# Kernel tuning notes

Hardware: AMD Instinct MI355X
Metric: run time of the kernel (lower is better)

Reference implementation:

```python
import jax, jax.numpy as jnp
import numpy as np

N_NODES = 100000
N_EDGES = 3200000
N_GRAPHS = 256
DIMS = [11, 200, 200, 200, 200, 200]  # acfg_init_dims + cfg_filters
CONCAT = sum(DIMS[1:])  # 1000


def setup_inputs() -> dict:
    key = jax.random.key(0)
    ks = jax.random.split(key, 32)
    d = {}
    d["x"] = jax.random.normal(ks[0], (N_NODES, DIMS[0]), jnp.float32)
    d["edge_index"] = jax.random.randint(ks[1], (2, N_EDGES), 0, N_NODES)
    d["batch"] = jnp.sort(jax.random.randint(ks[2], (N_NODES,), 0, N_GRAPHS))
    ki = 3
    # SAGEConv params: lin_l (neighbors, with bias) + lin_r (root, no bias)
    for i in range(5):
        fi, fo = DIMS[i], DIMS[i + 1]
        s = 1.0 / np.sqrt(fi)
        d[f"Wl{i+1}"] = jax.random.uniform(ks[ki], (fo, fi), jnp.float32, -s, s); ki += 1
        d[f"bl{i+1}"] = jnp.zeros((fo,), jnp.float32)
        d[f"Wr{i+1}"] = jax.random.uniform(ks[ki], (fo, fi), jnp.float32, -s, s); ki += 1
    # projection head 1000 -> 500 -> 250 -> 1
    for j, (fi, fo) in enumerate([(CONCAT, CONCAT // 2), (CONCAT // 2, CONCAT // 4), (CONCAT // 4, 1)]):
        s = 1.0 / np.sqrt(fi)
        d[f"pw{j+1}"] = jax.random.uniform(ks[ki], (fo, fi), jnp.float32, -s, s); ki += 1
        d[f"pb{j+1}"] = jnp.zeros((fo,), jnp.float32)
    return d


def reference(x, edge_index, batch,
              Wl1, bl1, Wr1, Wl2, bl2, Wr2, Wl3, bl3, Wr3,
              Wl4, bl4, Wr4, Wl5, bl5, Wr5,
              pw1, pb1, pw2, pb2, pw3, pb3):
    src, dst = edge_index[0], edge_index[1]
    # in-degree for mean aggregation (computed once, reused by all layers)
    deg = jax.ops.segment_sum(jnp.ones((src.shape[0],), x.dtype), dst, N_NODES)
    inv_deg = (1.0 / jnp.maximum(deg, 1.0))[:, None]

    def sage(h, Wl, bl, Wr):
        agg = jax.ops.segment_sum(h[src], dst, N_NODES) * inv_deg  # mean of neighbor feats
        return agg @ Wl.T + bl + h @ Wr.T

    layers = [(Wl1, bl1, Wr1), (Wl2, bl2, Wr2), (Wl3, bl3, Wr3), (Wl4, bl4, Wr4), (Wl5, bl5, Wr5)]
    h = x
    outs = []
    for Wl, bl, Wr in layers:
        h = jax.nn.relu(sage(h, Wl, bl, Wr))
        outs.append(h)
    hc = jnp.concatenate(outs, axis=1)  # [N, 1000]

    # global_mean_pool over graph ids
    cnt = jax.ops.segment_sum(jnp.ones((x.shape[0],), x.dtype), batch, N_GRAPHS)
    g = jax.ops.segment_sum(hc, batch, N_GRAPHS) / jnp.maximum(cnt, 1.0)[:, None]

    # dropout is identity in eval mode (functional.dropout with training=False)
    g = g @ pw1.T + pb1
    g = g @ pw2.T + pb2
    g = g @ pw3.T + pb3  # [num_graphs, 1]
    return jax.nn.sigmoid(g).squeeze(1)
```

## Files before the change

kernel.cpp:

```cpp
#include <hip/hip_runtime.h>
#include <math.h>

typedef __attribute__((ext_vector_type(4))) float floatx4;
typedef __attribute__((ext_vector_type(2))) float floatx2;

#define ROWP 256
#define R4   16
#define NT 14
#define NTC 13
#define KS 7
#define PACK_BYTES (NT*KS*64*8)
#define PACK1_BYTES (NT*64*8)
#define STAGE_BYTES (NTC*KS*64*8)
#define BSHIFT 6
#define EPB 4096
#define MAXBUCK 1600
#define PT_STRIDE 208

__device__ __forceinline__ unsigned short f2bf(float f){
    union { float f; unsigned u; } v; v.f = f;
    unsigned r = v.u + 0x7FFF + ((v.u >> 16) & 1);
    return (unsigned short)(r >> 16);
}
__device__ __forceinline__ unsigned pk4_fp8(float a, float b, float c, float d){
    int w = __builtin_amdgcn_cvt_pk_fp8_f32(a, b, 0, false);
    w = __builtin_amdgcn_cvt_pk_fp8_f32(c, d, w, true);
    return (unsigned)w;
}
__device__ __forceinline__ unsigned char b1_fp8(float a){
    int w = __builtin_amdgcn_cvt_pk_fp8_f32(a, a, 0, false);
    return (unsigned char)(w & 0xFF);
}


__global__ __launch_bounds__(256) void k_bin_hist(
    const int* __restrict__ dst, int* __restrict__ hist, int E, int nbuck)
{
    __shared__ int lh[MAXBUCK];
    for (int i = threadIdx.x; i < nbuck; i += 256) lh[i] = 0;
    __syncthreads();
    int base = blockIdx.x * EPB;
    #pragma unroll
    for (int k = 0; k < EPB / 256; ++k){
        int e = base + k * 256 + threadIdx.x;
        if (e < E) atomicAdd(&lh[dst[e] >> BSHIFT], 1);
    }
    __syncthreads();
    for (int i = threadIdx.x; i < nbuck; i += 256)
        hist[(size_t)blockIdx.x * nbuck + i] = lh[i];
}

__global__ __launch_bounds__(256) void k_col_scan(
    int* __restrict__ hist, int* __restrict__ T, int nblk, int nbuck)
{
    __shared__ int part[4][64];
    int w = threadIdx.x >> 6, l = threadIdx.x & 63;
    int b = blockIdx.x * 64 + l;
    int chunk = (nblk + 3) >> 2;
    int j0 = w * chunk, j1 = j0 + chunk; if (j1 > nblk) j1 = nblk;
    int s = 0;
    if (b < nbuck)
        for (int j = j0; j < j1; ++j) s += hist[(size_t)j * nbuck + b];
    part[w][l] = s;
    __syncthreads();
    if (b < nbuck){
        int run = 0;
        for (int w2 = 0; w2 < w; ++w2) run += part[w2][l];
        for (int j = j0; j < j1; ++j){
            int v = hist[(size_t)j * nbuck + b];
            hist[(size_t)j * nbuck + b] = run;
            run += v;
        }
        if (w == 3) T[b] = part[0][l] + part[1][l] + part[2][l] + part[3][l];
    }
}

__global__ __launch_bounds__(256) void k_scan_t(
    const int* __restrict__ T, int* __restrict__ tbase, int nbuck)
{
    __shared__ int ts[256];
    int t = threadIdx.x;
    int v[8]; int s = 0;
    int base = t * 8;
    #pragma unroll
    for (int k = 0; k < 8; ++k){
        int idx = base + k;
        v[k] = (idx < nbuck) ? T[idx] : 0;
        s += v[k];
    }
    ts[t] = s; __syncthreads();
    #pragma unroll
    for (int off = 1; off < 256; off <<= 1){
        int p = (t >= off) ? ts[t - off] : 0;
        __syncthreads();
        ts[t] += p;
        __syncthreads();
    }
    int run = ts[t] - s;
    #pragma unroll
    for (int k = 0; k < 8; ++k){
        int idx = base + k;
        if (idx < nbuck) tbase[idx] = run;
        run += v[k];
    }
    if (t == 255) tbase[nbuck] = ts[255];
}

__global__ __launch_bounds__(256) void k_bin_scatter(
    const int* __restrict__ src, const int* __restrict__ dst,
    const int* __restrict__ off, const int* __restrict__ tbase,
    unsigned* __restrict__ pairs, int E, int nbuck)
{
    __shared__ int lbase[MAXBUCK];
    __shared__ int lc[MAXBUCK];
    for (int i = threadIdx.x; i < nbuck; i += 256){
        lbase[i] = off[(size_t)blockIdx.x * nbuck + i] + tbase[i];
        lc[i] = 0;
    }
    __syncthreads();
    int base = blockIdx.x * EPB;
    #pragma unroll
    for (int k = 0; k < EPB / 256; ++k){
        int e = base + k * 256 + threadIdx.x;
        if (e < E){
            int d = dst[e];
            int b = d >> BSHIFT;
            int r = atomicAdd(&lc[b], 1);
            pairs[lbase[b] + r] = ((unsigned)(d & 63) << 26) | (unsigned)src[e];
        }
    }
}

__global__ __launch_bounds__(256) void k_bucket_deg(
    const unsigned* __restrict__ pairs, const int* __restrict__ tbase,
    int* __restrict__ deg, float* __restrict__ inv_deg, int N)
{
    __shared__ int ld[64];
    int b = blockIdx.x;
    if (threadIdx.x < 64) ld[threadIdx.x] = 0;
    __syncthreads();
    int pb = tbase[b], pe = tbase[b + 1];
    for (int e = pb + threadIdx.x; e < pe; e += 256)
        atomicAdd(&ld[pairs[e] >> 26], 1);
    __syncthreads();
    if (threadIdx.x < 64){
        int node = (b << BSHIFT) + threadIdx.x;
        if (node < N){
            int d = ld[threadIdx.x];
            deg[node] = d;
            inv_deg[node] = 1.0f / fmaxf((float)d, 1.0f);
        }
    }
}

__global__ __launch_bounds__(256) void k_place(
    const unsigned* __restrict__ pairs, const int* __restrict__ tbase,
    const int* __restrict__ row_ptr, int* __restrict__ srcs, int N)
{
    __shared__ int lrp[64];
    __shared__ int lcur[64];
    int b = blockIdx.x;
    if (threadIdx.x < 64){
        int node = (b << BSHIFT) + threadIdx.x;
        lrp[threadIdx.x] = (node < N) ? row_ptr[node] : 0;
        lcur[threadIdx.x] = 0;
    }
    __syncthreads();
    int pb = tbase[b], pe = tbase[b + 1];
    for (int e = pb + threadIdx.x; e < pe; e += 256){
        unsigned pr = pairs[e];
        int li = pr >> 26;
        int r = atomicAdd(&lcur[li], 1);
        srcs[lrp[li] + r] = (int)(pr & 0x03FFFFFFu);
    }
}


__global__ void k_scan_sums(const int* __restrict__ deg, int* __restrict__ csum, int N){
    __shared__ int sd[256];
    int base = blockIdx.x * 1024;
    int s = 0;
    for (int i = threadIdx.x; i < 1024; i += 256){
        int idx = base + i;
        s += (idx < N) ? deg[idx] : 0;
    }
    sd[threadIdx.x] = s; __syncthreads();
    for (int off = 128; off > 0; off >>= 1){
        if (threadIdx.x < off) sd[threadIdx.x] += sd[threadIdx.x + off];
        __syncthreads();
    }
    if (threadIdx.x == 0) csum[blockIdx.x] = sd[0];
}

__global__ void k_scan_apply(const int* __restrict__ deg, const int* __restrict__ csum,
                             int* __restrict__ row_ptr, int N, int E, int nchunks){
    __shared__ int ts[256];
    __shared__ int base_s;
    int partial = 0;
    for (int j = threadIdx.x; j < nchunks; j += 256)
        if (j < (int)blockIdx.x) partial += csum[j];
    ts[threadIdx.x] = partial; __syncthreads();
    for (int off = 128; off > 0; off >>= 1){
        if (threadIdx.x < off) ts[threadIdx.x] += ts[threadIdx.x + off];
        __syncthreads();
    }
    if (threadIdx.x == 0) base_s = ts[0];
    __syncthreads();
    int blk_base = base_s;
    __syncthreads();

    int base = blockIdx.x * 1024 + threadIdx.x * 4;
    int v[4]; int s = 0;
    #pragma unroll
    for (int j = 0; j < 4; ++j){
        int idx = base + j;
        v[j] = (idx < N) ? deg[idx] : 0;
        s += v[j];
    }
    ts[threadIdx.x] = s; __syncthreads();
    #pragma unroll
    for (int off = 1; off < 256; off <<= 1){
        int t = (threadIdx.x >= off) ? ts[threadIdx.x - off] : 0;
        __syncthreads();
        ts[threadIdx.x] += t;
        __syncthreads();
    }
    int excl = ts[threadIdx.x] - s + blk_base;
    #pragma unroll
    for (int j = 0; j < 4; ++j){
        int idx = base + j;
        if (idx < N) row_ptr[idx] = excl;
        excl += v[j];
    }
    if (blockIdx.x == 0 && threadIdx.x == 0) row_ptr[N] = E;
}


__global__ void k_gstart_bs(const int* __restrict__ batch, int* __restrict__ gstart,
                            int N, int NG){
    int g = blockIdx.x * blockDim.x + threadIdx.x;
    if (g > NG) return;
    int lo = 0, hi = N;
    while (lo < hi){
        int mid = (lo + hi) >> 1;
        if (batch[mid] < g) lo = mid + 1; else hi = mid;
    }
    gstart[g] = lo;
}


__global__ void k_pack_w(const float* W0, const float* W1, const float* W2, const float* W3,
                         const float* W4, const float* W5, const float* W6, const float* W7,
                         unsigned char* __restrict__ out){
    const float* Ws[8] = {W0,W1,W2,W3,W4,W5,W6,W7};
    const float* W = Ws[blockIdx.z];
    int lane = threadIdx.x;
    int n  = blockIdx.x * 16 + (lane & 15);
    int k0 = blockIdx.y * 32 + (lane >> 4) * 8;
    float f[8];
    #pragma unroll
    for (int j = 0; j < 8; ++j){
        int k = k0 + j;
        f[j] = (n < 200 && k < 200) ? W[n * 200 + k] : 0.f;
    }
    uint2 u;
    u.x = pk4_fp8(f[0], f[1], f[2], f[3]);
    u.y = pk4_fp8(f[4], f[5], f[6], f[7]);
    size_t off = ((((size_t)blockIdx.z * NT + blockIdx.x) * KS + blockIdx.y) * 64 + lane) * 8;
    *reinterpret_cast<uint2*>(out + off) = u;
}

__global__ __launch_bounds__(256) void k_pack_misc(
    const float* __restrict__ x, unsigned short* __restrict__ xp,
    unsigned char* __restrict__ xa,
    const float* __restrict__ Wl1, const float* __restrict__ Wr1,
    unsigned char* __restrict__ w1pack,
    const float* b0, const float* b1, const float* b2, const float* b3, const float* b4,
    float* __restrict__ biasp, int N, int xblk)
{
    int bid = blockIdx.x;
    if (bid < xblk){
        int i = bid * 256 + threadIdx.x;
        int node = i >> 4, c = i & 15;
        if (node < N){
            float f = (c < 11) ? x[(size_t)node * 11 + c] : 0.f;
            xp[i] = f2bf(f);
            xa[(size_t)node * 32 + 16 + c] = b1_fp8(f);
        }
        return;
    }
    int j = bid - xblk;
    if (j < NT){
        if (threadIdx.x >= 64) return;
        int lane = threadIdx.x;
        int n  = j * 16 + (lane & 15);
        int k0 = (lane >> 4) * 8;
        float f[8];
        #pragma unroll
        for (int jj = 0; jj < 8; ++jj){
            int k = k0 + jj;
            float v = 0.f;
            if (n < 200){
                if (k < 11)                 v = Wl1[n * 11 + k];
                else if (k >= 16 && k < 27) v = Wr1[n * 11 + (k - 16)];
            }
            f[jj] = v;
        }
        uint2 u;
        u.x = pk4_fp8(f[0], f[1], f[2], f[3]);
        u.y = pk4_fp8(f[4], f[5], f[6], f[7]);
        size_t off = ((size_t)j * 64 + lane) * 8;
        *reinterpret_cast<uint2*>(w1pack + off) = u;
        return;
    }
    int l = j - NT;
    const float* bs[5] = {b0,b1,b2,b3,b4};
    int c = threadIdx.x;
    if (c < ROWP) biasp[l * ROWP + c] = (c < 200) ? bs[l][c] : 0.f;
}


__global__ __launch_bounds__(256) void k_agg11(
    const unsigned short* __restrict__ xp, const int* __restrict__ row_ptr,
    const int* __restrict__ srcs, const float* __restrict__ inv_deg,
    unsigned char* __restrict__ xa, int N)
{
    int half = threadIdx.x >> 5;
    int node = blockIdx.x * 8 + half;
    int l = threadIdx.x & 31;
    if (node >= N) return;
    int beg = row_ptr[node], end = row_ptr[node + 1];

    float acc[12];
    #pragma unroll
    for (int i = 0; i < 12; ++i) acc[i] = 0.f;

    const uint4* x4 = reinterpret_cast<const uint4*>(xp);
    const uint2* x2 = reinterpret_cast<const uint2*>(xp);
    for (int e = beg + l; e < end; e += 32){
        int sn = srcs[e];
        uint4 a = x4[(size_t)sn * 2];
        uint2 b = x2[(size_t)sn * 4 + 2];
        union { unsigned u; float f; } c;
        c.u = a.x << 16;         acc[0] += c.f;
        c.u = a.x & 0xffff0000u; acc[1] += c.f;
        c.u = a.y << 16;         acc[2] += c.f;
        c.u = a.y & 0xffff0000u; acc[3] += c.f;
        c.u = a.z << 16;         acc[4] += c.f;
        c.u = a.z & 0xffff0000u; acc[5] += c.f;
        c.u = a.w << 16;         acc[6] += c.f;
        c.u = a.w & 0xffff0000u; acc[7] += c.f;
        c.u = b.x << 16;         acc[8] += c.f;
        c.u = b.x & 0xffff0000u; acc[9] += c.f;
        c.u = b.y << 16;         acc[10] += c.f;
        c.u = b.y & 0xffff0000u; acc[11] += c.f;
    }

    #pragma unroll
    for (int i = 0; i < 11; ++i){
        acc[i] += __shfl_xor(acc[i], 1, 64);
        acc[i] += __shfl_xor(acc[i], 2, 64);
        acc[i] += __shfl_xor(acc[i], 4, 64);
        acc[i] += __shfl_xor(acc[i], 8, 64);
        acc[i] += __shfl_xor(acc[i], 16, 64);
    }

    if (l == 0){
        float id = inv_deg[node];
        float v[12];
        #pragma unroll
        for (int i = 0; i < 11; ++i) v[i] = acc[i] * id;
        v[11] = 0.f;
        uint4 o;
        o.x = pk4_fp8(v[0], v[1], v[2], v[3]);
        o.y = pk4_fp8(v[4], v[5], v[6], v[7]);
        o.z = pk4_fp8(v[8], v[9], v[10], v[11]);
        o.w = 0u;
        *reinterpret_cast<uint4*>(xa + (size_t)node * 32) = o;
    }
}


__device__ __forceinline__ void accum_fp8v(floatx2* a, uint4 u){
    a[0] += __builtin_amdgcn_cvt_pk_f32_fp8((int)u.x, false);
    a[1] += __builtin_amdgcn_cvt_pk_f32_fp8((int)u.x, true );
    a[2] += __builtin_amdgcn_cvt_pk_f32_fp8((int)u.y, false);
    a[3] += __builtin_amdgcn_cvt_pk_f32_fp8((int)u.y, true );
    a[4] += __builtin_amdgcn_cvt_pk_f32_fp8((int)u.z, false);
    a[5] += __builtin_amdgcn_cvt_pk_f32_fp8((int)u.z, true );
    a[6] += __builtin_amdgcn_cvt_pk_f32_fp8((int)u.w, false);
    a[7] += __builtin_amdgcn_cvt_pk_f32_fp8((int)u.w, true );
}

__global__ __launch_bounds__(256) void k_agg200(
    const unsigned char* __restrict__ h8, const int* __restrict__ row_ptr,
    const int* __restrict__ srcs, const float* __restrict__ inv_deg,
    unsigned char* __restrict__ agg, int N)
{
    int node = blockIdx.x * 4 + (threadIdx.x >> 6);
    int lane = threadIdx.x & 63;
    if (node >= N) return;
    int g = lane >> 4;
    int l = lane & 15;
    int beg = row_ptr[node], end = row_ptr[node + 1];
    int nb = end - beg;

    floatx2 acc[8];
    #pragma unroll
    for (int i = 0; i < 8; ++i) acc[i] = (floatx2){0.f, 0.f};

    const uint4* h4 = reinterpret_cast<const uint4*>(h8);

    for (int t = 0; t < nb; t += 64){
        int cnt = nb - t; if (cnt > 64) cnt = 64;
        int eidx = t + lane;
        int si = srcs[beg + (eidx < nb ? eidx : nb - 1)];
        int jmax = (cnt - g + 3) >> 2;

        int j = 0;
        for (; j + 4 <= jmax; j += 4){
            int b0 = g + 4 * j;
            int s0 = __shfl(si, b0,      64);
            int s1 = __shfl(si, b0 + 4,  64);
            int s2 = __shfl(si, b0 + 8,  64);
            int s3 = __shfl(si, b0 + 12, 64);
            uint4 u0 = h4[(size_t)s0 * R4 + l];
            uint4 u1 = h4[(size_t)s1 * R4 + l];
            uint4 u2 = h4[(size_t)s2 * R4 + l];
            uint4 u3 = h4[(size_t)s3 * R4 + l];
            accum_fp8v(acc, u0);
            accum_fp8v(acc, u1);
            accum_fp8v(acc, u2);
            accum_fp8v(acc, u3);
        }
        for (; j < jmax; ++j){
            int s0 = __shfl(si, g + 4 * j, 64);
            uint4 u0 = h4[(size_t)s0 * R4 + l];
            accum_fp8v(acc, u0);
        }
    }

    float af[16];
    #pragma unroll
    for (int i = 0; i < 8; ++i){ af[2*i] = acc[i][0]; af[2*i+1] = acc[i][1]; }
    #pragma unroll
    for (int i = 0; i < 16; ++i){
        af[i] += __shfl_xor(af[i], 32, 64);
        af[i] += __shfl_xor(af[i], 16, 64);
    }

    if (g == 0){
        float id = inv_deg[node];
        uint4 o;
        o.x = pk4_fp8(af[0] * id,  af[1] * id,  af[2] * id,  af[3] * id);
        o.y = pk4_fp8(af[4] * id,  af[5] * id,  af[6] * id,  af[7] * id);
        o.z = pk4_fp8(af[8] * id,  af[9] * id,  af[10] * id, af[11] * id);
        o.w = pk4_fp8(af[12] * id, af[13] * id, af[14] * id, af[15] * id);
        *reinterpret_cast<uint4*>(agg + (size_t)node * ROWP + l * 16) = o;
    }
}


__global__ __launch_bounds__(256) void k_layer1_mfma(
    const unsigned char* __restrict__ xa, const unsigned char* __restrict__ W1p,
    const float* __restrict__ biasp, const int* __restrict__ batch,
    float* __restrict__ gsum, unsigned char* __restrict__ outp, int M)
{
    __shared__ __align__(16) unsigned char ptile[64 * PT_STRIDE];
    __shared__ int lb[64];
    const int wave = threadIdx.x >> 6;
    const int lane = threadIdx.x & 63;
    const int n = lane & 15;
    const int q = lane >> 4;
    const int r0 = blockIdx.x * 64;
    const int nrows = (M - r0 < 64) ? (M - r0) : 64;
    int row = r0 + wave * 16 + n;
    int rowc = row < M ? row : (M - 1);

    if (threadIdx.x < 64 && threadIdx.x < nrows) lb[threadIdx.x] = batch[r0 + threadIdx.x];

    long a = *reinterpret_cast<const long*>(xa + (size_t)rowc * 32 + q * 8);

    floatx4 acc[NTC];
    #pragma unroll
    for (int nt = 0; nt < NTC; ++nt){
        long b = *reinterpret_cast<const long*>(W1p + ((size_t)nt * 64 + lane) * 8);
        acc[nt] = __builtin_amdgcn_mfma_f32_16x16x32_fp8_fp8(a, b, (floatx4){0.f,0.f,0.f,0.f}, 0, 0, 0);
    }

    {
        int lr0 = wave * 16 + q * 4;
        #pragma unroll
        for (int nt = 0; nt < NTC; ++nt){
            float bsv = biasp[nt * 16 + n];
            #pragma unroll
            for (int r = 0; r < 4; ++r){
                float v = fmaxf(acc[nt][r] + bsv, 0.f);
                ptile[(lr0 + r) * PT_STRIDE + nt * 16 + n] = b1_fp8(v);
            }
        }
    }
    __syncthreads();

    {
        const uint4* s4 = reinterpret_cast<const uint4*>(ptile);
        int tot = nrows * 13;
        for (int i = threadIdx.x; i < tot; i += 256){
            int r = i / 13, c = i - r * 13;
            *reinterpret_cast<uint4*>(outp + (size_t)(r0 + r) * ROWP + c * 16) = s4[i];
        }
    }

    if (threadIdx.x < 50){
        int t = threadIdx.x;
        const unsigned* pd = reinterpret_cast<const unsigned*>(ptile);
        float s0 = 0.f, s1 = 0.f, s2 = 0.f, s3 = 0.f;
        int cur = lb[0];
        for (int r = 0; r < nrows; ++r){
            int gg = lb[r];
            if (gg != cur){
                float* gp = &gsum[(size_t)cur * 1000 + t * 4];
                atomicAdd(gp + 0, s0); atomicAdd(gp + 1, s1);
                atomicAdd(gp + 2, s2); atomicAdd(gp + 3, s3);
                s0 = s1 = s2 = s3 = 0.f;
                cur = gg;
            }
            unsigned u = pd[r * 52 + t];
            floatx2 lo = __builtin_amdgcn_cvt_pk_f32_fp8((int)u, false);
            floatx2 hi = __builtin_amdgcn_cvt_pk_f32_fp8((int)u, true);
            s0 += lo[0]; s1 += lo[1]; s2 += hi[0]; s3 += hi[1];
        }
        float* gp = &gsum[(size_t)cur * 1000 + t * 4];
        atomicAdd(gp + 0, s0); atomicAdd(gp + 1, s1);
        atomicAdd(gp + 2, s2); atomicAdd(gp + 3, s3);
    }
}

__global__ __launch_bounds__(256) void k_sage_mfma(
    const unsigned char* __restrict__ Aagg, const unsigned char* __restrict__ Ah,
    const unsigned char* __restrict__ Wlp, const unsigned char* __restrict__ Wrp,
    const float* __restrict__ biasp, const int* __restrict__ batch,
    float* __restrict__ gsum, int col_off,
    unsigned char* __restrict__ outp, int M)
{
    __shared__ __align__(16) unsigned char lw[STAGE_BYTES];
    __shared__ int lb[64];
    const int wave = threadIdx.x >> 6;
    const int lane = threadIdx.x & 63;
    const int n = lane & 15;
    const int q = lane >> 4;
    const int r0 = blockIdx.x * 64;
    const int nrows = (M - r0 < 64) ? (M - r0) : 64;
    int row = r0 + wave * 16 + n;
    int rowc = row < M ? row : (M - 1);

    if (threadIdx.x < 64 && threadIdx.x < nrows) lb[threadIdx.x] = batch[r0 + threadIdx.x];

    floatx4 acc[NTC];
    #pragma unroll
    for (int nt = 0; nt < NTC; ++nt) acc[nt] = (floatx4){0.f, 0.f, 0.f, 0.f};

    const unsigned char* Wp[2] = {Wlp, Wrp};
    const unsigned char* Ap[2] = {Aagg, Ah};

    #pragma unroll
    for (int phase = 0; phase < 2; ++phase){
        if (phase) __syncthreads();
        {
            const uint4* src4 = reinterpret_cast<const uint4*>(Wp[phase]);
            uint4* dst4 = reinterpret_cast<uint4*>(lw);
            for (int i = threadIdx.x; i < STAGE_BYTES / 16; i += 256)
                dst4[i] = src4[i];
        }
        __syncthreads();

        const unsigned char* arow = Ap[phase] + (size_t)rowc * ROWP + q * 8;
        long a[KS];
        #pragma unroll
        for (int ks = 0; ks < 6; ++ks)
            a[ks] = *reinterpret_cast<const long*>(arow + ks * 32);
        a[6] = (q < 2) ? *reinterpret_cast<const long*>(arow + 192) : 0L;

        #pragma unroll
        for (int ks = 0; ks < KS; ++ks){
            #pragma unroll
            for (int nt = 0; nt < NTC; ++nt){
                long b = *reinterpret_cast<const long*>(&lw[((nt * KS + ks) * 64 + lane) * 8]);
                acc[nt] = __builtin_amdgcn_mfma_f32_16x16x32_fp8_fp8(a[ks], b, acc[nt], 0, 0, 0);
            }
        }
    }
    __syncthreads();

    unsigned char* ptile = lw;
    {
        int lr0 = wave * 16 + q * 4;
        #pragma unroll
        for (int nt = 0; nt < NTC; ++nt){
            float bsv = biasp[nt * 16 + n];
            #pragma unroll
            for (int r = 0; r < 4; ++r){
                float v = fmaxf(acc[nt][r] + bsv, 0.f);
                ptile[(lr0 + r) * PT_STRIDE + nt * 16 + n] = b1_fp8(v);
            }
        }
    }
    __syncthreads();

    {
        const uint4* s4 = reinterpret_cast<const uint4*>(ptile);
        int tot = nrows * 13;
        for (int i = threadIdx.x; i < tot; i += 256){
            int r = i / 13, c = i - r * 13;
            *reinterpret_cast<uint4*>(outp + (size_t)(r0 + r) * ROWP + c * 16) = s4[i];
        }
    }

    if (threadIdx.x < 50){
        int t = threadIdx.x;
        const unsigned* pd = reinterpret_cast<const unsigned*>(ptile);
        float s0 = 0.f, s1 = 0.f, s2 = 0.f, s3 = 0.f;
        int cur = lb[0];
        for (int r = 0; r < nrows; ++r){
            int gg = lb[r];
            if (gg != cur){
                float* gp = &gsum[(size_t)cur * 1000 + col_off + t * 4];
                atomicAdd(gp + 0, s0); atomicAdd(gp + 1, s1);
                atomicAdd(gp + 2, s2); atomicAdd(gp + 3, s3);
                s0 = s1 = s2 = s3 = 0.f;
                cur = gg;
            }
            unsigned u = pd[r * 52 + t];
            floatx2 lo = __builtin_amdgcn_cvt_pk_f32_fp8((int)u, false);
            floatx2 hi = __builtin_amdgcn_cvt_pk_f32_fp8((int)u, true);
            s0 += lo[0]; s1 += lo[1]; s2 += hi[0]; s3 += hi[1];
        }
        float* gp = &gsum[(size_t)cur * 1000 + col_off + t * 4];
        atomicAdd(gp + 0, s0); atomicAdd(gp + 1, s1);
        atomicAdd(gp + 2, s2); atomicAdd(gp + 3, s3);
    }
}


__global__ __launch_bounds__(256) void k_mlp_first(
    const float* __restrict__ gsum, const int* __restrict__ gstart,
    const float* __restrict__ W, const float* __restrict__ b,
    float* __restrict__ outp)
{
    __shared__ __align__(16) float row[1000];
    int g = blockIdx.x;
    int cnt = gstart[g+1] - gstart[g];
    float inv = 1.0f / fmaxf((float)cnt, 1.0f);
    for (int i = threadIdx.x; i < 1000; i += 256)
        row[i] = gsum[(size_t)g * 1000 + i] * inv;
    __syncthreads();
    for (int c = threadIdx.x; c < 500; c += 256){
        const float4* w4 = reinterpret_cast<const float4*>(W + (size_t)c * 1000);
        const float4* r4 = reinterpret_cast<const float4*>(row);
        float s = b[c];
        for (int k = 0; k < 250; ++k){
            float4 wv = w4[k]; float4 rv = r4[k];
            s = fmaf(wv.x, rv.x, s);
            s = fmaf(wv.y, rv.y, s);
            s = fmaf(wv.z, rv.z, s);
            s = fmaf(wv.w, rv.w, s);
        }
        outp[(size_t)g * 500 + c] = s;
    }
}

__global__ __launch_bounds__(256) void k_mlp23(
    const float* __restrict__ t1, const float* __restrict__ W2,
    const float* __restrict__ b2, const float* __restrict__ W3,
    const float* __restrict__ b3, float* __restrict__ outp)
{
    __shared__ __align__(16) float row[500];
    __shared__ float red[256];
    int g = blockIdx.x;
    for (int i = threadIdx.x; i < 500; i += 256) row[i] = t1[(size_t)g * 500 + i];
    __syncthreads();
    float prod = 0.f;
    int c = threadIdx.x;
    if (c < 250){
        const float4* w4 = reinterpret_cast<const float4*>(W2 + (size_t)c * 500);
        const float4* r4 = reinterpret_cast<const float4*>(row);
        float s = b2[c];
        for (int k = 0; k < 125; ++k){
            float4 wv = w4[k]; float4 rv = r4[k];
            s = fmaf(wv.x, rv.x, s);
            s = fmaf(wv.y, rv.y, s);
            s = fmaf(wv.z, rv.z, s);
            s = fmaf(wv.w, rv.w, s);
        }
        prod = s * W3[c];
    }
    red[threadIdx.x] = prod;
    __syncthreads();
    for (int off = 128; off > 0; off >>= 1){
        if (threadIdx.x < off) red[threadIdx.x] += red[threadIdx.x + off];
        __syncthreads();
    }
    if (threadIdx.x == 0)
        outp[g] = 1.0f / (1.0f + expf(-(red[0] + b3[0])));
}


extern "C" void kernel_launch(void* const* d_in, const int* in_sizes, int n_in,
                              void* d_out, int out_size, void* d_ws, size_t ws_size,
                              hipStream_t stream)
{
    const float* x    = (const float*)d_in[0];
    const int*   ei   = (const int*)d_in[1];
    const int*   batch= (const int*)d_in[2];
    const float* Wl[5]; const float* bl[5]; const float* Wr[5];
    for (int i = 0; i < 5; ++i){
        Wl[i] = (const float*)d_in[3 + 3*i];
        bl[i] = (const float*)d_in[4 + 3*i];
        Wr[i] = (const float*)d_in[5 + 3*i];
    }
    const float* pw1 = (const float*)d_in[18]; const float* pb1 = (const float*)d_in[19];
    const float* pw2 = (const float*)d_in[20]; const float* pb2 = (const float*)d_in[21];
    const float* pw3 = (const float*)d_in[22]; const float* pb3 = (const float*)d_in[23];
    float* out = (float*)d_out;

    const int N  = in_sizes[2];
    const int E  = in_sizes[1] / 2;
    const int NG = out_size;
    const int* esrc = ei;
    const int* edst = ei + E;
    const int nbuck = (N + 63) >> BSHIFT;
    const int nblk  = (E + EPB - 1) / EPB;

    char* p = (char*)d_ws;
    auto carve = [&](size_t bytes)->void* {
        void* r = (void*)p;
        p += (bytes + 255) & ~(size_t)255;
        return r;
    };
    int*   deg     = (int*)  carve((size_t)N * 4);
    int*   row_ptr = (int*)  carve(((size_t)N + 1) * 4);
    int*   csum    = (int*)  carve(4096);
    int*   hist    = (int*)  carve((size_t)nblk * nbuck * 4);
    int*   Tb      = (int*)  carve((size_t)nbuck * 4);
    int*   tbase   = (int*)  carve(((size_t)nbuck + 1) * 4);
    float* invdeg  = (float*)carve((size_t)N * 4);
    int*   gstart  = (int*)  carve(((size_t)NG + 1) * 4);
    int*   srcs    = (int*)  carve((size_t)E * 4);
    unsigned* pairs = (unsigned*)carve((size_t)E * 4);
    unsigned short* xp    = (unsigned short*)carve((size_t)N * 16 * 2);
    unsigned char*  xa    = (unsigned char*) carve((size_t)N * 32);
    unsigned char*  agg8  = (unsigned char*) carve((size_t)N * ROWP);
    unsigned char*  h8A   = (unsigned char*) carve((size_t)N * ROWP);
    unsigned char*  h8B   = (unsigned char*) carve((size_t)N * ROWP);
    unsigned char*  wpack = (unsigned char*) carve((size_t)8 * PACK_BYTES);
    unsigned char*  w1pack= (unsigned char*) carve((size_t)PACK1_BYTES);
    float* biasp   = (float*)carve((size_t)5 * ROWP * 4);
    float* gsum    = (float*)carve((size_t)NG * 1000 * 4);
    float* t1      = (float*)carve((size_t)NG * 500 * 4);

    hipMemsetAsync(gsum, 0, (size_t)NG * 1000 * 4, stream);
    hipMemsetAsync(h8A, 0, (size_t)N * ROWP, stream);
    hipMemsetAsync(h8B, 0, (size_t)N * ROWP, stream);

    int xblk = (N * 16 + 255) / 256;
    k_pack_w<<<dim3(NT, KS, 8), 64, 0, stream>>>(
        Wl[1], Wr[1], Wl[2], Wr[2], Wl[3], Wr[3], Wl[4], Wr[4], wpack);
    k_pack_misc<<<xblk + NT + 5, 256, 0, stream>>>(
        x, xp, xa, Wl[0], Wr[0], w1pack,
        bl[0], bl[1], bl[2], bl[3], bl[4], biasp, N, xblk);

    k_bin_hist<<<nblk, 256, 0, stream>>>(edst, hist, E, nbuck);
    k_col_scan<<<(nbuck + 63) / 64, 256, 0, stream>>>(hist, Tb, nblk, nbuck);
    k_scan_t<<<1, 256, 0, stream>>>(Tb, tbase, nbuck);
    k_bin_scatter<<<nblk, 256, 0, stream>>>(esrc, edst, hist, tbase, pairs, E, nbuck);
    k_bucket_deg<<<nbuck, 256, 0, stream>>>(pairs, tbase, deg, invdeg, N);
    int nchunks = (N + 1023) / 1024;
    k_scan_sums<<<nchunks, 256, 0, stream>>>(deg, csum, N);
    k_scan_apply<<<nchunks, 256, 0, stream>>>(deg, csum, row_ptr, N, E, nchunks);
    k_place<<<nbuck, 256, 0, stream>>>(pairs, tbase, row_ptr, srcs, N);

    k_gstart_bs<<<(NG + 256) / 256, 256, 0, stream>>>(batch, gstart, N, NG);

    int gb = (N + 63) / 64;
    k_agg11<<<(N + 7) / 8, 256, 0, stream>>>(xp, row_ptr, srcs, invdeg, xa, N);
    k_layer1_mfma<<<gb, 256, 0, stream>>>(xa, w1pack, biasp, batch, gsum, h8A, N);

    unsigned char* hc = h8A; unsigned char* hn = h8B;
    int ab = (N + 3) / 4;
    for (int L = 1; L < 5; ++L){
        k_agg200<<<ab, 256, 0, stream>>>(hc, row_ptr, srcs, invdeg, agg8, N);
        const unsigned char* Wlp = wpack + (size_t)((L-1)*2 + 0) * PACK_BYTES;
        const unsigned char* Wrp = wpack + (size_t)((L-1)*2 + 1) * PACK_BYTES;
        k_sage_mfma<<<gb, 256, 0, stream>>>(agg8, hc, Wlp, Wrp,
                                            biasp + L * ROWP, batch, gsum, 200 * L,
                                            hn, N);
        k_pool_dummy:;
        unsigned char* t = hc; hc = hn; hn = t;
    }

    k_mlp_first<<<NG, 256, 0, stream>>>(gsum, gstart, pw1, pb1, t1);
    k_mlp23<<<NG, 256, 0, stream>>>(t1, pw2, pb2, pw3, pb3, out);
}
```

Baseline: 1.110 ms.

## Split fp8 feature rows into two 128-byte column planes for aggregation

Node feature and aggregate buffers move from one 256-byte row per node to two planes of 128 bytes each. Neighbor aggregation now runs as two launches, one per plane, with 8 lanes per edge and 8 edges in flight per wave instead of 16 and 4. The aim is a smaller gather working set per launch so more of it stays in cache. In exchange, `srcs`/`row_ptr` are read twice, there is an extra launch and reduction step, and the MFMA kernel now loads unmasked padding columns in plane 1.

```diff
diff --git a/kernel.cpp b/kernel.cpp
--- a/kernel.cpp
+++ b/kernel.cpp
@@ -5,7 +5,6 @@
 typedef __attribute__((ext_vector_type(2))) float floatx2;
 
 #define ROWP 256
-#define R4   16
 #define NT 14
 #define NTC 13
 #define KS 7
@@ -16,6 +15,7 @@
 #define EPB 4096
 #define MAXBUCK 1600
 #define PT_STRIDE 208
+
 
 __device__ __forceinline__ unsigned short f2bf(float f){
     union { float f; unsigned u; } v; v.f = f;
@@ -392,16 +392,16 @@
     a[7] += __builtin_amdgcn_cvt_pk_f32_fp8((int)u.w, true );
 }
 
-__global__ __launch_bounds__(256) void k_agg200(
-    const unsigned char* __restrict__ h8, const int* __restrict__ row_ptr,
+__global__ __launch_bounds__(256) void k_agg200h(
+    const unsigned char* __restrict__ hpl, const int* __restrict__ row_ptr,
     const int* __restrict__ srcs, const float* __restrict__ inv_deg,
-    unsigned char* __restrict__ agg, int N)
+    unsigned char* __restrict__ aggpl, int N)
 {
     int node = blockIdx.x * 4 + (threadIdx.x >> 6);
     int lane = threadIdx.x & 63;
     if (node >= N) return;
-    int g = lane >> 4;
-    int l = lane & 15;
+    int g = lane >> 3;
+    int l = lane & 7;
     int beg = row_ptr[node], end = row_ptr[node + 1];
     int nb = end - beg;
 
@@ -409,33 +409,33 @@
     #pragma unroll
     for (int i = 0; i < 8; ++i) acc[i] = (floatx2){0.f, 0.f};
 
-    const uint4* h4 = reinterpret_cast<const uint4*>(h8);
+    const uint4* h4 = reinterpret_cast<const uint4*>(hpl);
 
     for (int t = 0; t < nb; t += 64){
         int cnt = nb - t; if (cnt > 64) cnt = 64;
         int eidx = t + lane;
         int si = srcs[beg + (eidx < nb ? eidx : nb - 1)];
-        int jmax = (cnt - g + 3) >> 2;
+        int jmax = (cnt - g + 7) >> 3;
 
         int j = 0;
         for (; j + 4 <= jmax; j += 4){
-            int b0 = g + 4 * j;
+            int b0 = g + 8 * j;
             int s0 = __shfl(si, b0,      64);
-            int s1 = __shfl(si, b0 + 4,  64);
-            int s2 = __shfl(si, b0 + 8,  64);
-            int s3 = __shfl(si, b0 + 12, 64);
-            uint4 u0 = h4[(size_t)s0 * R4 + l];
-            uint4 u1 = h4[(size_t)s1 * R4 + l];
-            uint4 u2 = h4[(size_t)s2 * R4 + l];
-            uint4 u3 = h4[(size_t)s3 * R4 + l];
+            int s1 = __shfl(si, b0 + 8,  64);
+            int s2 = __shfl(si, b0 + 16, 64);
+            int s3 = __shfl(si, b0 + 24, 64);
+            uint4 u0 = h4[(size_t)s0 * 8 + l];
+            uint4 u1 = h4[(size_t)s1 * 8 + l];
+            uint4 u2 = h4[(size_t)s2 * 8 + l];
+            uint4 u3 = h4[(size_t)s3 * 8 + l];
             accum_fp8v(acc, u0);
             accum_fp8v(acc, u1);
             accum_fp8v(acc, u2);
             accum_fp8v(acc, u3);
         }
         for (; j < jmax; ++j){
-            int s0 = __shfl(si, g + 4 * j, 64);
-            uint4 u0 = h4[(size_t)s0 * R4 + l];
+            int s0 = __shfl(si, g + 8 * j, 64);
+            uint4 u0 = h4[(size_t)s0 * 8 + l];
             accum_fp8v(acc, u0);
         }
     }
@@ -445,8 +445,9 @@
     for (int i = 0; i < 8; ++i){ af[2*i] = acc[i][0]; af[2*i+1] = acc[i][1]; }
     #pragma unroll
     for (int i = 0; i < 16; ++i){
+        af[i] += __shfl_xor(af[i], 8, 64);
+        af[i] += __shfl_xor(af[i], 16, 64);
         af[i] += __shfl_xor(af[i], 32, 64);
-        af[i] += __shfl_xor(af[i], 16, 64);
     }
 
     if (g == 0){
@@ -456,7 +457,7 @@
         o.y = pk4_fp8(af[4] * id,  af[5] * id,  af[6] * id,  af[7] * id);
         o.z = pk4_fp8(af[8] * id,  af[9] * id,  af[10] * id, af[11] * id);
         o.w = pk4_fp8(af[12] * id, af[13] * id, af[14] * id, af[15] * id);
-        *reinterpret_cast<uint4*>(agg + (size_t)node * ROWP + l * 16) = o;
+        *reinterpret_cast<uint4*>(aggpl + (size_t)node * 128 + l * 16) = o;
     }
 }
 
@@ -503,11 +504,16 @@
     __syncthreads();
 
     {
+        unsigned char* out0 = outp;
+        unsigned char* out1 = outp + (size_t)M * 128;
         const uint4* s4 = reinterpret_cast<const uint4*>(ptile);
         int tot = nrows * 13;
         for (int i = threadIdx.x; i < tot; i += 256){
             int r = i / 13, c = i - r * 13;
-            *reinterpret_cast<uint4*>(outp + (size_t)(r0 + r) * ROWP + c * 16) = s4[i];
+            unsigned char* dst = (c < 8)
+                ? out0 + (size_t)(r0 + r) * 128 + c * 16
+                : out1 + (size_t)(r0 + r) * 128 + (c - 8) * 16;
+            *reinterpret_cast<uint4*>(dst) = s4[i];
         }
     }
 
@@ -562,6 +568,7 @@
 
     const unsigned char* Wp[2] = {Wlp, Wrp};
     const unsigned char* Ap[2] = {Aagg, Ah};
+    const size_t plane = (size_t)M * 128;
 
     #pragma unroll
     for (int phase = 0; phase < 2; ++phase){
@@ -574,12 +581,15 @@
         }
         __syncthreads();
 
-        const unsigned char* arow = Ap[phase] + (size_t)rowc * ROWP + q * 8;
+        const unsigned char* A0 = Ap[phase] + (size_t)rowc * 128 + q * 8;
+        const unsigned char* A1 = A0 + plane;
         long a[KS];
         #pragma unroll
-        for (int ks = 0; ks < 6; ++ks)
-            a[ks] = *reinterpret_cast<const long*>(arow + ks * 32);
-        a[6] = (q < 2) ? *reinterpret_cast<const long*>(arow + 192) : 0L;
+        for (int ks = 0; ks < 4; ++ks)
+            a[ks] = *reinterpret_cast<const long*>(A0 + ks * 32);
+        #pragma unroll
+        for (int ks = 4; ks < KS; ++ks)
+            a[ks] = *reinterpret_cast<const long*>(A1 + (ks - 4) * 32);
 
         #pragma unroll
         for (int ks = 0; ks < KS; ++ks){
@@ -608,11 +618,16 @@
     __syncthreads();
 
     {
+        unsigned char* out0 = outp;
+        unsigned char* out1 = outp + plane;
         const uint4* s4 = reinterpret_cast<const uint4*>(ptile);
         int tot = nrows * 13;
         for (int i = threadIdx.x; i < tot; i += 256){
             int r = i / 13, c = i - r * 13;
-            *reinterpret_cast<uint4*>(outp + (size_t)(r0 + r) * ROWP + c * 16) = s4[i];
+            unsigned char* dst = (c < 8)
+                ? out0 + (size_t)(r0 + r) * 128 + c * 16
+                : out1 + (size_t)(r0 + r) * 128 + (c - 8) * 16;
+            *reinterpret_cast<uint4*>(dst) = s4[i];
         }
     }
 
@@ -787,14 +802,15 @@
 
     unsigned char* hc = h8A; unsigned char* hn = h8B;
     int ab = (N + 3) / 4;
+    size_t plane = (size_t)N * 128;
     for (int L = 1; L < 5; ++L){
-        k_agg200<<<ab, 256, 0, stream>>>(hc, row_ptr, srcs, invdeg, agg8, N);
+        k_agg200h<<<ab, 256, 0, stream>>>(hc,         row_ptr, srcs, invdeg, agg8,         N);
+        k_agg200h<<<ab, 256, 0, stream>>>(hc + plane, row_ptr, srcs, invdeg, agg8 + plane, N);
         const unsigned char* Wlp = wpack + (size_t)((L-1)*2 + 0) * PACK_BYTES;
         const unsigned char* Wrp = wpack + (size_t)((L-1)*2 + 1) * PACK_BYTES;
         k_sage_mfma<<<gb, 256, 0, stream>>>(agg8, hc, Wlp, Wrp,
                                             biasp + L * ROWP, batch, gsum, 200 * L,
                                             hn, N);
-        k_pool_dummy:;
         unsigned char* t = hc; hc = hn; hn = t;
     }
 
```

Measured after the change: 1.389 ms. +25.1%, slower.

## Split node features into 32-byte column planes and gather per slice

Applied to the files above, without the earlier changes.

Stores the fp8 node feature rows as eight planes of 32 bytes per node instead of one 256-byte row. The aggregation kernel now gives each block one plane for 128 nodes and two threads per node, each walking that node's neighbor list on its own, instead of one wave per node with shuffles. The aim is a smaller gather working set per plane and no cross-lane reductions. In exchange it adds thread divergence from uneven degrees and gathers an eighth plane that is not needed. It also reads padding bytes that are never written and that the old code explicitly zeroed.

```diff
diff --git a/kernel.cpp b/kernel.cpp
--- a/kernel.cpp
+++ b/kernel.cpp
@@ -5,7 +5,6 @@
 typedef __attribute__((ext_vector_type(2))) float floatx2;
 
 #define ROWP 256
-#define R4   16
 #define NT 14
 #define NTC 13
 #define KS 7
@@ -16,6 +15,7 @@
 #define EPB 4096
 #define MAXBUCK 1600
 #define PT_STRIDE 208
+
 
 __device__ __forceinline__ unsigned short f2bf(float f){
     union { float f; unsigned u; } v; v.f = f;
@@ -392,72 +392,53 @@
     a[7] += __builtin_amdgcn_cvt_pk_f32_fp8((int)u.w, true );
 }
 
-__global__ __launch_bounds__(256) void k_agg200(
-    const unsigned char* __restrict__ h8, const int* __restrict__ row_ptr,
+__global__ __launch_bounds__(256) void k_agg200s(
+    const unsigned char* __restrict__ hpl, const int* __restrict__ row_ptr,
     const int* __restrict__ srcs, const float* __restrict__ inv_deg,
-    unsigned char* __restrict__ agg, int N)
-{
-    int node = blockIdx.x * 4 + (threadIdx.x >> 6);
-    int lane = threadIdx.x & 63;
+    unsigned char* __restrict__ aggpl, int N)
+{
+    const int s    = blockIdx.x & 7;
+    const int nb0  = (blockIdx.x >> 3) * 128;
+    const int grp  = threadIdx.x >> 1;
+    const int half = threadIdx.x & 1;
+    const int node = nb0 + grp;
     if (node >= N) return;
-    int g = lane >> 4;
-    int l = lane & 15;
+    const size_t plane = (size_t)N * 32;
+    const uint4* h4 = reinterpret_cast<const uint4*>(hpl + (size_t)s * plane);
     int beg = row_ptr[node], end = row_ptr[node + 1];
-    int nb = end - beg;
 
     floatx2 acc[8];
     #pragma unroll
     for (int i = 0; i < 8; ++i) acc[i] = (floatx2){0.f, 0.f};
 
-    const uint4* h4 = reinterpret_cast<const uint4*>(h8);
-
-    for (int t = 0; t < nb; t += 64){
-        int cnt = nb - t; if (cnt > 64) cnt = 64;
-        int eidx = t + lane;
-        int si = srcs[beg + (eidx < nb ? eidx : nb - 1)];
-        int jmax = (cnt - g + 3) >> 2;
-
-        int j = 0;
-        for (; j + 4 <= jmax; j += 4){
-            int b0 = g + 4 * j;
-            int s0 = __shfl(si, b0,      64);
-            int s1 = __shfl(si, b0 + 4,  64);
-            int s2 = __shfl(si, b0 + 8,  64);
-            int s3 = __shfl(si, b0 + 12, 64);
-            uint4 u0 = h4[(size_t)s0 * R4 + l];
-            uint4 u1 = h4[(size_t)s1 * R4 + l];
-            uint4 u2 = h4[(size_t)s2 * R4 + l];
-            uint4 u3 = h4[(size_t)s3 * R4 + l];
-            accum_fp8v(acc, u0);
-            accum_fp8v(acc, u1);
-            accum_fp8v(acc, u2);
-            accum_fp8v(acc, u3);
-        }
-        for (; j < jmax; ++j){
-            int s0 = __shfl(si, g + 4 * j, 64);
-            uint4 u0 = h4[(size_t)s0 * R4 + l];
-            accum_fp8v(acc, u0);
-        }
-    }
-
-    float af[16];
-    #pragma unroll
-    for (int i = 0; i < 8; ++i){ af[2*i] = acc[i][0]; af[2*i+1] = acc[i][1]; }
-    #pragma unroll
-    for (int i = 0; i < 16; ++i){
-        af[i] += __shfl_xor(af[i], 32, 64);
-        af[i] += __shfl_xor(af[i], 16, 64);
-    }
-
-    if (g == 0){
-        float id = inv_deg[node];
-        uint4 o;
-        o.x = pk4_fp8(af[0] * id,  af[1] * id,  af[2] * id,  af[3] * id);
-        o.y = pk4_fp8(af[4] * id,  af[5] * id,  af[6] * id,  af[7] * id);
-        o.z = pk4_fp8(af[8] * id,  af[9] * id,  af[10] * id, af[11] * id);
-        o.w = pk4_fp8(af[12] * id, af[13] * id, af[14] * id, af[15] * id);
-        *reinterpret_cast<uint4*>(agg + (size_t)node * ROWP + l * 16) = o;
-    }
+    int e = beg;
+    for (; e + 4 <= end; e += 4){
+        int s0 = srcs[e];
+        int s1 = srcs[e + 1];
+        int s2 = srcs[e + 2];
+        int s3 = srcs[e + 3];
+        uint4 u0 = h4[(size_t)s0 * 2 + half];
+        uint4 u1 = h4[(size_t)s1 * 2 + half];
+        uint4 u2 = h4[(size_t)s2 * 2 + half];
+        uint4 u3 = h4[(size_t)s3 * 2 + half];
+        accum_fp8v(acc, u0);
+        accum_fp8v(acc, u1);
+        accum_fp8v(acc, u2);
+        accum_fp8v(acc, u3);
+    }
+    for (; e < end; ++e){
+        int s0 = srcs[e];
+        uint4 u0 = h4[(size_t)s0 * 2 + half];
+        accum_fp8v(acc, u0);
+    }
+
+    float id = inv_deg[node];
+    uint4 o;
+    o.x = pk4_fp8(acc[0][0]*id, acc[0][1]*id, acc[1][0]*id, acc[1][1]*id);
+    o.y = pk4_fp8(acc[2][0]*id, acc[2][1]*id, acc[3][0]*id, acc[3][1]*id);
+    o.z = pk4_fp8(acc[4][0]*id, acc[4][1]*id, acc[5][0]*id, acc[5][1]*id);
+    o.w = pk4_fp8(acc[6][0]*id, acc[6][1]*id, acc[7][0]*id, acc[7][1]*id);
+    *reinterpret_cast<uint4*>(aggpl + (size_t)s * plane + (size_t)node * 32 + half * 16) = o;
 }
 
 
@@ -503,11 +484,14 @@
     __syncthreads();
 
     {
+        const size_t plane = (size_t)M * 32;
         const uint4* s4 = reinterpret_cast<const uint4*>(ptile);
         int tot = nrows * 13;
         for (int i = threadIdx.x; i < tot; i += 256){
             int r = i / 13, c = i - r * 13;
-            *reinterpret_cast<uint4*>(outp + (size_t)(r0 + r) * ROWP + c * 16) = s4[i];
+            unsigned char* dst = outp + (size_t)(c >> 1) * plane
+                               + (size_t)(r0 + r) * 32 + (c & 1) * 16;
+            *reinterpret_cast<uint4*>(dst) = s4[i];
         }
     }
 
@@ -562,6 +546,7 @@
 
     const unsigned char* Wp[2] = {Wlp, Wrp};
     const unsigned char* Ap[2] = {Aagg, Ah};
+    const size_t plane = (size_t)M * 32;
 
     #pragma unroll
     for (int phase = 0; phase < 2; ++phase){
@@ -574,12 +559,11 @@
         }
         __syncthreads();
 
-        const unsigned char* arow = Ap[phase] + (size_t)rowc * ROWP + q * 8;
+        const unsigned char* Ab = Ap[phase] + (size_t)rowc * 32 + q * 8;
         long a[KS];
         #pragma unroll
-        for (int ks = 0; ks < 6; ++ks)
-            a[ks] = *reinterpret_cast<const long*>(arow + ks * 32);
-        a[6] = (q < 2) ? *reinterpret_cast<const long*>(arow + 192) : 0L;
+        for (int ks = 0; ks < KS; ++ks)
+            a[ks] = *reinterpret_cast<const long*>(Ab + (size_t)ks * plane);
 
         #pragma unroll
         for (int ks = 0; ks < KS; ++ks){
@@ -612,7 +596,9 @@
         int tot = nrows * 13;
         for (int i = threadIdx.x; i < tot; i += 256){
             int r = i / 13, c = i - r * 13;
-            *reinterpret_cast<uint4*>(outp + (size_t)(r0 + r) * ROWP + c * 16) = s4[i];
+            unsigned char* dst = outp + (size_t)(c >> 1) * plane
+                               + (size_t)(r0 + r) * 32 + (c & 1) * 16;
+            *reinterpret_cast<uint4*>(dst) = s4[i];
         }
     }
 
@@ -786,15 +772,14 @@
     k_layer1_mfma<<<gb, 256, 0, stream>>>(xa, w1pack, biasp, batch, gsum, h8A, N);
 
     unsigned char* hc = h8A; unsigned char* hn = h8B;
-    int ab = (N + 3) / 4;
+    int gs = ((N + 127) / 128) * 8;
     for (int L = 1; L < 5; ++L){
-        k_agg200<<<ab, 256, 0, stream>>>(hc, row_ptr, srcs, invdeg, agg8, N);
+        k_agg200s<<<gs, 256, 0, stream>>>(hc, row_ptr, srcs, invdeg, agg8, N);
         const unsigned char* Wlp = wpack + (size_t)((L-1)*2 + 0) * PACK_BYTES;
         const unsigned char* Wrp = wpack + (size_t)((L-1)*2 + 1) * PACK_BYTES;
         k_sage_mfma<<<gb, 256, 0, stream>>>(agg8, hc, Wlp, Wrp,
                                             biasp + L * ROWP, batch, gsum, 200 * L,
                                             hn, N);
-        k_pool_dummy:;
         unsigned char* t = hc; hc = hn; hn = t;
     }
 
```

Result: slower. 1.364 ms (+22.9%).
